# Performance work log

Hardware: AMD Instinct MI355X
Metric: run time of the kernel (lower is better)

## Reference

```python
import jax, jax.numpy as jnp
import numpy as np

B, S, D, H = 2, 2048, 1024, 16
HD = D // H  # head_dim = 64
ROPE_BASE = 10000.0
INIT_STD = 0.02


def setup_inputs() -> dict:
    key = jax.random.key(0)
    k1, k2, k3 = jax.random.split(key, 3)
    x = jax.random.normal(k1, (B, S, D), dtype=jnp.float32)
    w_qkv = jax.random.normal(k2, (3 * D, D), dtype=jnp.float32) * INIT_STD
    w_out = jax.random.normal(k3, (D, D), dtype=jnp.float32) * (1.0 / np.sqrt(D))
    b_out = jnp.zeros((D,), dtype=jnp.float32)
    return {"x": x, "w_qkv": w_qkv, "w_out": w_out, "b_out": b_out}


def _rope_cos_sin(s_len, head_dim, dtype):
    theta = 1.0 / ROPE_BASE ** (jnp.arange(0, head_dim, 2, dtype=jnp.float32) / head_dim)
    freqs = jnp.outer(jnp.arange(s_len, dtype=jnp.float32), theta)  # [s, d/2]
    freqs = jnp.concatenate([freqs, freqs], axis=-1)  # [s, d]
    return jnp.cos(freqs).astype(dtype), jnp.sin(freqs).astype(dtype)


def _apply_rope(qk, cos, sin):
    # qk: [b, h, s, d]; rotate-half: (-x2, x1)
    d2 = qk.shape[-1] // 2
    x1, x2 = qk[..., :d2], qk[..., d2:]
    rot = jnp.concatenate([-x2, x1], axis=-1)
    return qk * cos + rot * sin


def reference(x, w_qkv, w_out, b_out):
    b, s, d = x.shape
    qkv = jnp.einsum('bsd,ed->bse', x, w_qkv)  # [b, s, 3D]
    qkv = qkv.reshape(b, s, 3 * H, HD).transpose(0, 2, 1, 3)  # [b, 3h, s, d]
    qk, v = qkv[:, :2 * H], qkv[:, 2 * H:]
    cos, sin = _rope_cos_sin(s, HD, x.dtype)
    qk = _apply_rope(qk, cos, sin)
    q, k = qk[:, :H], qk[:, H:]
    scale = 1.0 / np.sqrt(HD)
    scores = jnp.einsum('bhqd,bhkd->bhqk', q, k) * scale  # [b, h, s, s]
    causal = jnp.tril(jnp.ones((s, s), dtype=bool))
    scores = jnp.where(causal, scores, jnp.finfo(scores.dtype).min)
    attn = jax.nn.softmax(scores, axis=-1)
    o = jnp.einsum('bhqk,bhkd->bhqd', attn, v)  # [b, h, s, d]
    o = o.transpose(0, 2, 1, 3).reshape(b, s, d)
    return jnp.einsum('bsd,ed->bse', o, w_out) + b_out
```

## Files before the change

### kernel.cpp

```cpp
#include <hip/hip_runtime.h>
#include <hip/hip_fp16.h>
#include <math.h>

#define B_  2
#define S_  2048
#define D_  1024
#define H_  16
#define HD_ 64

typedef _Float16  f16;
typedef __attribute__((ext_vector_type(8))) _Float16 f16x8;
typedef __attribute__((ext_vector_type(4))) _Float16 f16x4;
typedef __attribute__((ext_vector_type(4))) float    f32x4;

#define LOG2E 1.4426950408889634f
#define L2_10000_DIV32 0.41524101186092029f
#define PS 72

__device__ __forceinline__ float fin(float v) { return (v == v) ? v : 0.0f; }

__device__ __forceinline__ f16x8 cvt8(const float* p) {
  float4 a = *(const float4*)p;
  float4 b = *(const float4*)(p + 4);
  f16x8 h;
  h[0] = (f16)a.x; h[1] = (f16)a.y; h[2] = (f16)a.z; h[3] = (f16)a.w;
  h[4] = (f16)b.x; h[5] = (f16)b.y; h[6] = (f16)b.z; h[7] = (f16)b.w;
  return h;
}

__device__ __forceinline__ int swz64(int r, int c) {
  return r * 64 + ((((c >> 3) ^ (r & 7)) << 3) | (c & 7));
}

__global__ void __launch_bounds__(256)
k_cvt3(const float* __restrict__ wq, const float* __restrict__ wo,
       const float* __restrict__ x,
       f16* __restrict__ wqh, f16* __restrict__ woh, f16* __restrict__ xh,
       int doX)
{
  const int NWQ = 3 * D_ * D_ / 4, NWO = D_ * D_ / 4, NX = B_ * S_ * D_ / 4;
  const int n = NWQ + NWO + (doX ? NX : 0);
  for (int i = blockIdx.x * 256 + threadIdx.x; i < n; i += gridDim.x * 256) {
    const float* src; f16* dst; int j;
    if (i < NWQ)            { src = wq; dst = wqh; j = i; }
    else if (i < NWQ + NWO) { src = wo; dst = woh; j = i - NWQ; }
    else                    { src = x;  dst = xh;  j = i - NWQ - NWO; }
    float4 v = ((const float4*)src)[j];
    f16x4 h = {(f16)v.x, (f16)v.y, (f16)v.z, (f16)v.w};
    ((f16x4*)dst)[j] = h;
  }
}

template <bool XF16>
__global__ void __launch_bounds__(256)
k_qkv3(const float* __restrict__ xf, const f16* __restrict__ xh,
       const f16* __restrict__ wqh,
       f16* __restrict__ Qb, f16* __restrict__ Kb, f16* __restrict__ Vt)
{
  __shared__ __align__(16) f16 As[128 * PS];
  __shared__ __align__(16) f16 Bs[128 * PS];
  const int t = threadIdx.x;
  const int w = t >> 6;
  const int lane = t & 63;
  const int ll = lane & 15;
  const int quad = lane >> 4;
  const int wm = w >> 1, wn = w & 1;
  const int row0 = blockIdx.y * 128;
  const int col0 = blockIdx.x * 128;

  const f32x4 fz = {0.f, 0.f, 0.f, 0.f};
  f32x4 acc[4][4];
#pragma unroll
  for (int i = 0; i < 4; ++i)
#pragma unroll
    for (int j = 0; j < 4; ++j) acc[i][j] = fz;

  const int ldr = t >> 3;
  const int ldk = (t & 7) * 8;
  const float* gaf = xf  + (size_t)(row0 + ldr) * D_ + ldk;
  const f16*   gah = xh  + (size_t)(row0 + ldr) * D_ + ldk;
  const f16*   gb  = wqh + (size_t)(col0 + ldr) * D_ + ldk;

  for (int kt = 0; kt < D_; kt += 64) {
    f16x8 ra[4], rb[4];
#pragma unroll
    for (int i = 0; i < 4; ++i) {
      ra[i] = XF16 ? *(const f16x8*)(gah + (size_t)i * 32 * D_ + kt)
                   : cvt8(gaf + (size_t)i * 32 * D_ + kt);
      rb[i] = *(const f16x8*)(gb + (size_t)i * 32 * D_ + kt);
    }
    __syncthreads();
#pragma unroll
    for (int i = 0; i < 4; ++i) {
      *(f16x8*)&As[(i * 32 + ldr) * PS + ldk] = ra[i];
      *(f16x8*)&Bs[(i * 32 + ldr) * PS + ldk] = rb[i];
    }
    __syncthreads();
#pragma unroll
    for (int kk = 0; kk < 64; kk += 32) {
      f16x8 a[4], b[4];
#pragma unroll
      for (int mt = 0; mt < 4; ++mt)
        a[mt] = *(const f16x8*)&As[(wm * 64 + mt * 16 + ll) * PS + kk + quad * 8];
#pragma unroll
      for (int nt = 0; nt < 4; ++nt)
        b[nt] = *(const f16x8*)&Bs[(wn * 64 + nt * 16 + ll) * PS + kk + quad * 8];
#pragma unroll
      for (int mt = 0; mt < 4; ++mt)
#pragma unroll
        for (int nt = 0; nt < 4; ++nt)
          acc[mt][nt] = __builtin_amdgcn_mfma_f32_16x16x32_f16(
              a[mt], b[nt], acc[mt][nt], 0, 0, 0);
    }
  }

  const int h3 = (col0 >> 6) + wn;
  if (h3 < 32) {
    f16* dst = (h3 < 16) ? Qb : Kb;
    const int h = (h3 < 16) ? h3 : h3 - 16;
    const float th0 = exp2f(-(float)ll * L2_10000_DIV32);
    const float th1 = exp2f(-(float)(16 + ll) * L2_10000_DIV32);
#pragma unroll
    for (int mt = 0; mt < 4; ++mt) {
#pragma unroll
      for (int r = 0; r < 4; ++r) {
        const int row = row0 + wm * 64 + mt * 16 + quad * 4 + r;
        const int b = row >> 11;
        const int p = row & (S_ - 1);
        f16* base = dst + ((size_t)(b * H_ + h) * S_ + p) * HD_;
        const float fp = (float)p;
        float s0, c0, s1, c1;
        sincosf(fp * th0, &s0, &c0);
        sincosf(fp * th1, &s1, &c1);
        {
          float x1 = acc[mt][0][r], x2 = acc[mt][2][r];
          base[ll]      = (f16)fin(x1 * c0 - x2 * s0);
          base[ll + 32] = (f16)fin(x2 * c0 + x1 * s0);
        }
        {
          float x1 = acc[mt][1][r], x2 = acc[mt][3][r];
          base[16 + ll]      = (f16)fin(x1 * c1 - x2 * s1);
          base[16 + ll + 32] = (f16)fin(x2 * c1 + x1 * s1);
        }
      }
    }
  } else {
    const int hv = h3 - 32;
#pragma unroll
    for (int mt = 0; mt < 4; ++mt)
#pragma unroll
      for (int nt = 0; nt < 4; ++nt)
#pragma unroll
        for (int r = 0; r < 4; ++r) {
          const int row = row0 + wm * 64 + mt * 16 + quad * 4 + r;
          const int b = row >> 11;
          const int p = row & (S_ - 1);
          const int dd = nt * 16 + ll;
          Vt[((size_t)(b * H_ + hv) * HD_ + dd) * S_ + p] = (f16)fin(acc[mt][nt][r]);
        }
  }
}

__device__ __forceinline__ bool softmax_tile4(
    f32x4 sc[4], bool diag, int qloc, int ll, int quad,
    float& mrun, float& lrun, float& alpha, f16* Pt)
{
  if (diag) {
#pragma unroll
    for (int nt = 0; nt < 4; ++nt)
#pragma unroll
      for (int r = 0; r < 4; ++r)
        if ((nt * 16 + quad * 4 + r) > qloc) sc[nt][r] = -3.0e4f;
  }
  float pm = mrun;
#pragma unroll
  for (int nt = 0; nt < 4; ++nt)
#pragma unroll
    for (int r = 0; r < 4; ++r) pm = fmaxf(pm, sc[nt][r]);
  pm = fmaxf(pm, __shfl_xor(pm, 16));
  pm = fmaxf(pm, __shfl_xor(pm, 32));
  const bool resc = !__all(pm <= mrun + 8.0f);
  if (resc) { alpha = exp2f(mrun - pm); mrun = pm; }
  float ps = 0.f;
#pragma unroll
  for (int nt = 0; nt < 4; ++nt) {
    f16x4 pk;
#pragma unroll
    for (int r = 0; r < 4; ++r) {
      float p = exp2f(sc[nt][r] - mrun);
      ps += p;
      pk[r] = (f16)p;
    }
    *(f16x4*)&Pt[swz64(ll, nt * 16 + quad * 4)] = pk;
  }
  ps += __shfl_xor(ps, 16);
  ps += __shfl_xor(ps, 32);
  lrun = (resc ? lrun * alpha : lrun) + ps;
  return resc;
}

__device__ __forceinline__ void write_o4(
    f32x4 acco[4], float lrun, f16* Pt, int ll, int quad, int w,
    int qt, size_t bh, f16* Ob)
{
  const float inv = 1.0f / fmaxf(lrun, 1e-30f);
#pragma unroll
  for (int dg = 0; dg < 4; ++dg) {
    f16x4 ov;
#pragma unroll
    for (int r = 0; r < 4; ++r) ov[r] = (f16)fin(acco[dg][r] * inv);
    *(f16x4*)&Pt[swz64(ll, dg * 16 + quad * 4)] = ov;
  }
#pragma unroll
  for (int s2 = 0; s2 < 2; ++s2) {
    f16x8 o = *(const f16x8*)&Pt[swz64(ll, (quad + 4 * s2) * 8)];
    const size_t row = bh * S_ + qt * 64 + w * 16 + ll;
    *(f16x8*)&Ob[row * HD_ + (quad + 4 * s2) * 8] = o;
  }
}

__global__ void __launch_bounds__(256, 4)
k_attn4(const f16* Qb, const f16* __restrict__ Kb,
        const f16* __restrict__ Vt, f16* Ob)
{
  __shared__ __align__(16) f16 Ks[2][64 * 64];
  __shared__ __align__(16) f16 Vs[2][64 * 64];
  __shared__ __align__(16) f16 Ps[4][16 * 64];

  const int t = threadIdx.x;
  const int w = t >> 6;
  const int lane = t & 63;
  const int ll = lane & 15;
  const int quad = lane >> 4;
  const int bx = blockIdx.x;
  const int base = (bx & 1) ? 31 - (bx >> 1) : (bx >> 1);
  const int qt = ((int)blockIdx.y < 8) ? base : 31 - base;
  const int h = blockIdx.y;
  const int b = blockIdx.z;
  const size_t bh = (size_t)b * H_ + h;
  const f16* Qg = Qb + bh * S_ * HD_;
  const f16* Kg = Kb + bh * S_ * HD_;
  const f16* Vg = Vt + bh * HD_ * S_;

  f16x8 bq[2];
  {
    const f16 hsc = (f16)(0.125f * LOG2E);
#pragma unroll
    for (int k2 = 0; k2 < 2; ++k2) {
      bq[k2] = *(const f16x8*)(Qg + (size_t)(qt * 64 + w * 16 + ll) * HD_ + k2 * 32 + quad * 8);
#pragma unroll
      for (int e = 0; e < 8; ++e) bq[k2][e] *= hsc;
    }
  }
  const int sr = t >> 2;
  const int scc = (t & 3) * 16;
  {
    f16x8 a0 = *(const f16x8*)(Kg + (size_t)sr * HD_ + scc);
    f16x8 a1 = *(const f16x8*)(Kg + (size_t)sr * HD_ + scc + 8);
    f16x8 b0 = *(const f16x8*)(Vg + (size_t)sr * S_ + scc);
    f16x8 b1 = *(const f16x8*)(Vg + (size_t)sr * S_ + scc + 8);
    *(f16x8*)&Ks[0][swz64(sr, scc)]     = a0;
    *(f16x8*)&Ks[0][swz64(sr, scc + 8)] = a1;
    *(f16x8*)&Vs[0][swz64(sr, scc)]     = b0;
    *(f16x8*)&Vs[0][swz64(sr, scc + 8)] = b1;
  }
  __syncthreads();

  const f32x4 fz = {0.f, 0.f, 0.f, 0.f};
  f32x4 acco[4] = {fz, fz, fz, fz};
  float m = -3.0e4f, l = 0.f;
  const int qloc = w * 16 + ll;
  f16* Pt = &Ps[w][0];

  for (int kt = 0; kt <= qt; ++kt) {
    const int cur = kt & 1;
    const bool pre = (kt < qt);
    f16x8 nk0, nk1, nv0, nv1;
    if (pre) {
      const int kn = (kt + 1) * 64;
      nk0 = *(const f16x8*)(Kg + (size_t)(kn + sr) * HD_ + scc);
      nk1 = *(const f16x8*)(Kg + (size_t)(kn + sr) * HD_ + scc + 8);
      nv0 = *(const f16x8*)(Vg + (size_t)sr * S_ + kn + scc);
      nv1 = *(const f16x8*)(Vg + (size_t)sr * S_ + kn + scc + 8);
    }
    const f16* Kc = Ks[cur];
    const f16* Vc = Vs[cur];

    f16x8 ak[2][4];
#pragma unroll
    for (int k2 = 0; k2 < 2; ++k2)
#pragma unroll
      for (int nt = 0; nt < 4; ++nt)
        ak[k2][nt] = *(const f16x8*)&Kc[swz64(nt * 16 + ll, k2 * 32 + quad * 8)];

    f32x4 s[4] = {fz, fz, fz, fz};
#pragma unroll
    for (int k2 = 0; k2 < 2; ++k2)
#pragma unroll
      for (int nt = 0; nt < 4; ++nt)
        s[nt] = __builtin_amdgcn_mfma_f32_16x16x32_f16(ak[k2][nt], bq[k2], s[nt], 0, 0, 0);

    f16x8 av[2][4];
#pragma unroll
    for (int k2 = 0; k2 < 2; ++k2)
#pragma unroll
      for (int dg = 0; dg < 4; ++dg)
        av[k2][dg] = *(const f16x8*)&Vc[swz64(dg * 16 + ll, k2 * 32 + quad * 8)];

    float alpha;
    const bool resc = softmax_tile4(s, kt == qt, qloc, ll, quad, m, l, alpha, Pt);
    if (resc) {
#pragma unroll
      for (int dg = 0; dg < 4; ++dg)
#pragma unroll
        for (int r = 0; r < 4; ++r) acco[dg][r] *= alpha;
    }
#pragma unroll
    for (int k2 = 0; k2 < 2; ++k2) {
      f16x8 bp = *(const f16x8*)&Pt[swz64(ll, k2 * 32 + quad * 8)];
#pragma unroll
      for (int dg = 0; dg < 4; ++dg)
        acco[dg] = __builtin_amdgcn_mfma_f32_16x16x32_f16(av[k2][dg], bp, acco[dg], 0, 0, 0);
    }

    if (pre) {
      *(f16x8*)&Ks[1 - cur][swz64(sr, scc)]     = nk0;
      *(f16x8*)&Ks[1 - cur][swz64(sr, scc + 8)] = nk1;
      *(f16x8*)&Vs[1 - cur][swz64(sr, scc)]     = nv0;
      *(f16x8*)&Vs[1 - cur][swz64(sr, scc + 8)] = nv1;
    }
    __syncthreads();
  }

  write_o4(acco, l, Pt, ll, quad, w, qt, bh, Ob);
}

__global__ void __launch_bounds__(256)
k_out3(const f16* __restrict__ Ob, const f16* __restrict__ Wh,
       const float* __restrict__ bias, float* __restrict__ out)
{
  __shared__ __align__(16) f16 As[64 * PS];
  __shared__ __align__(16) f16 Bs[128 * PS];
  const int t = threadIdx.x;
  const int w = t >> 6;
  const int lane = t & 63;
  const int ll = lane & 15;
  const int quad = lane >> 4;
  const int wm = w >> 1, wn = w & 1;
  const int row0 = blockIdx.y * 64;
  const int col0 = blockIdx.x * 128;
  const int bb = row0 >> 11;
  const int s0 = row0 & (S_ - 1);

  const f32x4 fz = {0.f, 0.f, 0.f, 0.f};
  f32x4 acc[2][4];
#pragma unroll
  for (int i = 0; i < 2; ++i)
#pragma unroll
    for (int j = 0; j < 4; ++j) acc[i][j] = fz;

  const int ldr = t >> 3;
  const int ldk = (t & 7) * 8;
  const f16* gb = Wh + (size_t)(col0 + ldr) * D_ + ldk;

  for (int kt = 0; kt < 16; ++kt) {
    const f16* ga = Ob + (((size_t)(bb * H_ + kt)) * S_ + s0 + ldr) * HD_ + ldk;
    f16x8 ra[2], rb[4];
#pragma unroll
    for (int i = 0; i < 2; ++i)
      ra[i] = *(const f16x8*)(ga + (size_t)i * 32 * HD_);
#pragma unroll
    for (int i = 0; i < 4; ++i)
      rb[i] = *(const f16x8*)(gb + (size_t)i * 32 * D_ + kt * 64);
    __syncthreads();
#pragma unroll
    for (int i = 0; i < 2; ++i)
      *(f16x8*)&As[(i * 32 + ldr) * PS + ldk] = ra[i];
#pragma unroll
    for (int i = 0; i < 4; ++i)
      *(f16x8*)&Bs[(i * 32 + ldr) * PS + ldk] = rb[i];
    __syncthreads();
#pragma unroll
    for (int kk = 0; kk < 64; kk += 32) {
      f16x8 a[2], b[4];
#pragma unroll
      for (int mt = 0; mt < 2; ++mt)
        a[mt] = *(const f16x8*)&As[(wm * 32 + mt * 16 + ll) * PS + kk + quad * 8];
#pragma unroll
      for (int nt = 0; nt < 4; ++nt)
        b[nt] = *(const f16x8*)&Bs[(wn * 64 + nt * 16 + ll) * PS + kk + quad * 8];
#pragma unroll
      for (int mt = 0; mt < 2; ++mt)
#pragma unroll
        for (int nt = 0; nt < 4; ++nt)
          acc[mt][nt] = __builtin_amdgcn_mfma_f32_16x16x32_f16(
              a[mt], b[nt], acc[mt][nt], 0, 0, 0);
    }
  }

#pragma unroll
  for (int mt = 0; mt < 2; ++mt)
#pragma unroll
    for (int r = 0; r < 4; ++r) {
      const int row = row0 + wm * 32 + mt * 16 + quad * 4 + r;
#pragma unroll
      for (int nt = 0; nt < 4; ++nt) {
        const int col = col0 + wn * 64 + nt * 16 + ll;
        out[(size_t)row * D_ + col] = fin(acc[mt][nt][r] + bias[col]);
      }
    }
}

extern "C" void kernel_launch(void* const* d_in, const int* in_sizes, int n_in,
                              void* d_out, int out_size, void* d_ws, size_t ws_size,
                              hipStream_t stream) {
  const float* x    = (const float*)d_in[0];
  const float* wqkv = (const float*)d_in[1];
  const float* wout = (const float*)d_in[2];
  const float* bout = (const float*)d_in[3];
  float* out = (float*)d_out;

  char* ws = (char*)d_ws;
  f16* wqh = (f16*)(ws);
  f16* Qb  = (f16*)(ws + 6291456);
  f16* Kb  = (f16*)(ws + 14680064);
  f16* Vt  = (f16*)(ws + 23068672);
  f16* woh = (f16*)(ws + 31457280);
  const bool bigws = ws_size >= (size_t)41943040;
  f16* xh  = (f16*)(ws + 33554432);

  k_cvt3<<<2048, 256, 0, stream>>>(wqkv, wout, x, wqh, woh, xh, bigws ? 1 : 0);
  if (bigws)
    k_qkv3<true><<<dim3(3 * D_ / 128, (B_ * S_) / 128), 256, 0, stream>>>(
        x, xh, wqh, Qb, Kb, Vt);
  else
    k_qkv3<false><<<dim3(3 * D_ / 128, (B_ * S_) / 128), 256, 0, stream>>>(
        x, xh, wqh, Qb, Kb, Vt);
  k_attn4<<<dim3(32, H_, B_), 256, 0, stream>>>(Qb, Kb, Vt, Qb );
  k_out3<<<dim3(D_ / 128, (B_ * S_) / 64), 256, 0, stream>>>(
      Qb, woh, bout, out);
}
```

Measured before the change: 183.0 us.

## Use direct global-to-LDS loads with XOR-swizzled tiles in QKV and output GEMMs

Replaces the register-staged global→register→LDS tile copies in the QKV projection and output projection GEMMs with global_load_lds (16-byte direct-to-LDS) transfers. The LDS layout switches from padded rows (stride 72) to an unpadded 64-wide XOR swizzle, with the global source column permuted per lane so the swizzle is still applied. This removes VGPR staging and LDS write instructions and shrinks shared memory. In exchange, the loads are no longer issued before the first barrier, so global latency is no longer overlapped with the previous iteration's barrier wait.

```diff
diff --git a/kernel.cpp b/kernel.cpp
--- a/kernel.cpp
+++ b/kernel.cpp
@@ -15,7 +15,6 @@
 
 #define LOG2E 1.4426950408889634f
 #define L2_10000_DIV32 0.41524101186092029f
-#define PS 72
 
 __device__ __forceinline__ float fin(float v) { return (v == v) ? v : 0.0f; }
 
@@ -31,6 +30,11 @@
 __device__ __forceinline__ int swz64(int r, int c) {
   return r * 64 + ((((c >> 3) ^ (r & 7)) << 3) | (c & 7));
 }
+
+#define GLD16(g, l)                                                        \
+  __builtin_amdgcn_global_load_lds(                                        \
+      (const __attribute__((address_space(1))) void*)(g),                  \
+      (__attribute__((address_space(3))) void*)(l), 16, 0, 0)
 
 __global__ void __launch_bounds__(256)
 k_cvt3(const float* __restrict__ wq, const float* __restrict__ wo,
@@ -57,8 +61,8 @@
        const f16* __restrict__ wqh,
        f16* __restrict__ Qb, f16* __restrict__ Kb, f16* __restrict__ Vt)
 {
-  __shared__ __align__(16) f16 As[128 * PS];
-  __shared__ __align__(16) f16 Bs[128 * PS];
+  __shared__ __align__(16) f16 As[128 * 64];
+  __shared__ __align__(16) f16 Bs[128 * 64];
   const int t = threadIdx.x;
   const int w = t >> 6;
   const int lane = t & 63;
@@ -75,25 +79,35 @@
 #pragma unroll
     for (int j = 0; j < 4; ++j) acc[i][j] = fz;
 
+  const int rO = lane >> 3;
+  const int gc = (lane & 7) ^ rO;
+  const f16* gah2 = xh  + (size_t)(row0 + w * 8 + rO) * D_ + gc * 8;
+  const f16* gb2  = wqh + (size_t)(col0 + w * 8 + rO) * D_ + gc * 8;
+
   const int ldr = t >> 3;
   const int ldk = (t & 7) * 8;
-  const float* gaf = xf  + (size_t)(row0 + ldr) * D_ + ldk;
-  const f16*   gah = xh  + (size_t)(row0 + ldr) * D_ + ldk;
-  const f16*   gb  = wqh + (size_t)(col0 + ldr) * D_ + ldk;
+  const float* gaf = xf + (size_t)(row0 + ldr) * D_ + ldk;
 
   for (int kt = 0; kt < D_; kt += 64) {
-    f16x8 ra[4], rb[4];
-#pragma unroll
-    for (int i = 0; i < 4; ++i) {
-      ra[i] = XF16 ? *(const f16x8*)(gah + (size_t)i * 32 * D_ + kt)
-                   : cvt8(gaf + (size_t)i * 32 * D_ + kt);
-      rb[i] = *(const f16x8*)(gb + (size_t)i * 32 * D_ + kt);
+    f16x8 ra[4];
+    if (!XF16) {
+#pragma unroll
+      for (int i = 0; i < 4; ++i)
+        ra[i] = cvt8(gaf + (size_t)i * 32 * D_ + kt);
     }
     __syncthreads();
-#pragma unroll
-    for (int i = 0; i < 4; ++i) {
-      *(f16x8*)&As[(i * 32 + ldr) * PS + ldk] = ra[i];
-      *(f16x8*)&Bs[(i * 32 + ldr) * PS + ldk] = rb[i];
+    if (XF16) {
+#pragma unroll
+      for (int i = 0; i < 4; ++i) {
+        GLD16(gah2 + (size_t)(i * 32) * D_ + kt, &As[(i * 32 + w * 8) * 64]);
+        GLD16(gb2  + (size_t)(i * 32) * D_ + kt, &Bs[(i * 32 + w * 8) * 64]);
+      }
+    } else {
+#pragma unroll
+      for (int i = 0; i < 4; ++i) {
+        *(f16x8*)&As[swz64(i * 32 + ldr, ldk)] = ra[i];
+        GLD16(gb2 + (size_t)(i * 32) * D_ + kt, &Bs[(i * 32 + w * 8) * 64]);
+      }
     }
     __syncthreads();
 #pragma unroll
@@ -101,10 +115,10 @@
       f16x8 a[4], b[4];
 #pragma unroll
       for (int mt = 0; mt < 4; ++mt)
-        a[mt] = *(const f16x8*)&As[(wm * 64 + mt * 16 + ll) * PS + kk + quad * 8];
+        a[mt] = *(const f16x8*)&As[swz64(wm * 64 + mt * 16 + ll, kk + quad * 8)];
 #pragma unroll
       for (int nt = 0; nt < 4; ++nt)
-        b[nt] = *(const f16x8*)&Bs[(wn * 64 + nt * 16 + ll) * PS + kk + quad * 8];
+        b[nt] = *(const f16x8*)&Bs[swz64(wn * 64 + nt * 16 + ll, kk + quad * 8)];
 #pragma unroll
       for (int mt = 0; mt < 4; ++mt)
 #pragma unroll
@@ -339,8 +353,8 @@
 k_out3(const f16* __restrict__ Ob, const f16* __restrict__ Wh,
        const float* __restrict__ bias, float* __restrict__ out)
 {
-  __shared__ __align__(16) f16 As[64 * PS];
-  __shared__ __align__(16) f16 Bs[128 * PS];
+  __shared__ __align__(16) f16 As[64 * 64];
+  __shared__ __align__(16) f16 Bs[128 * 64];
   const int t = threadIdx.x;
   const int w = t >> 6;
   const int lane = t & 63;
@@ -359,36 +373,29 @@
 #pragma unroll
     for (int j = 0; j < 4; ++j) acc[i][j] = fz;
 
-  const int ldr = t >> 3;
-  const int ldk = (t & 7) * 8;
-  const f16* gb = Wh + (size_t)(col0 + ldr) * D_ + ldk;
+  const int rO = lane >> 3;
+  const int gc = (lane & 7) ^ rO;
+  const f16* gb2 = Wh + (size_t)(col0 + w * 8 + rO) * D_ + gc * 8;
 
   for (int kt = 0; kt < 16; ++kt) {
-    const f16* ga = Ob + (((size_t)(bb * H_ + kt)) * S_ + s0 + ldr) * HD_ + ldk;
-    f16x8 ra[2], rb[4];
+    const f16* ga2 = Ob + (((size_t)(bb * H_ + kt)) * S_ + s0 + w * 8 + rO) * HD_ + gc * 8;
+    __syncthreads();
 #pragma unroll
     for (int i = 0; i < 2; ++i)
-      ra[i] = *(const f16x8*)(ga + (size_t)i * 32 * HD_);
+      GLD16(ga2 + (size_t)(i * 32) * HD_, &As[(i * 32 + w * 8) * 64]);
 #pragma unroll
     for (int i = 0; i < 4; ++i)
-      rb[i] = *(const f16x8*)(gb + (size_t)i * 32 * D_ + kt * 64);
-    __syncthreads();
-#pragma unroll
-    for (int i = 0; i < 2; ++i)
-      *(f16x8*)&As[(i * 32 + ldr) * PS + ldk] = ra[i];
-#pragma unroll
-    for (int i = 0; i < 4; ++i)
-      *(f16x8*)&Bs[(i * 32 + ldr) * PS + ldk] = rb[i];
+      GLD16(gb2 + (size_t)(i * 32) * D_ + kt * 64, &Bs[(i * 32 + w * 8) * 64]);
     __syncthreads();
 #pragma unroll
     for (int kk = 0; kk < 64; kk += 32) {
       f16x8 a[2], b[4];
 #pragma unroll
       for (int mt = 0; mt < 2; ++mt)
-        a[mt] = *(const f16x8*)&As[(wm * 32 + mt * 16 + ll) * PS + kk + quad * 8];
+        a[mt] = *(const f16x8*)&As[swz64(wm * 32 + mt * 16 + ll, kk + quad * 8)];
 #pragma unroll
       for (int nt = 0; nt < 4; ++nt)
-        b[nt] = *(const f16x8*)&Bs[(wn * 64 + nt * 16 + ll) * PS + kk + quad * 8];
+        b[nt] = *(const f16x8*)&Bs[swz64(wn * 64 + nt * 16 + ll, kk + quad * 8)];
 #pragma unroll
       for (int mt = 0; mt < 2; ++mt)
 #pragma unroll
```

After: 184.5 us. No clear change (+0.8%).
